# Kernel tuning notes

Measured on AMD Instinct MI355X. Metric: run time of the kernel, lower is better.

## Reference

```python
import jax, jax.numpy as jnp
import numpy as np

VOCAB = 1500   # vocab_size
NE = 208       # n_embed
T = 256        # block_size
NH = 4         # n_head
HD = NE // NH  # head_size = 52
NL = 8         # n_layer
B = 256        # batch


def setup_inputs() -> dict:
    key = jax.random.key(0)
    ks = jax.random.split(key, 16)
    f = lambda k, shape: jax.random.normal(k, shape, jnp.float32) * 0.02
    return {
        "idx": jax.random.randint(ks[0], (B, T), 0, VOCAB),
        "targets": jax.random.randint(ks[1], (B, T), 0, VOCAB),
        "tok_emb": f(ks[2], (VOCAB, NE)),
        "pos_emb": f(ks[3], (T, NE)),
        # per-layer stacked attention params (separate no-bias Q/K/V Linears per head)
        "Wq": f(ks[4], (NL, NH, NE, HD)),
        "Wk": f(ks[5], (NL, NH, NE, HD)),
        "Wv": f(ks[6], (NL, NH, NE, HD)),
        "Wo": f(ks[7], (NL, NE, NE)),
        "bo": jnp.zeros((NL, NE), jnp.float32),
        "ln1_g": jnp.ones((NL, NE), jnp.float32),
        "ln1_b": jnp.zeros((NL, NE), jnp.float32),
        "W1": f(ks[8], (NL, NE, 4 * NE)),
        "b1": jnp.zeros((NL, 4 * NE), jnp.float32),
        "W2": f(ks[9], (NL, 4 * NE, NE)),
        "b2": jnp.zeros((NL, NE), jnp.float32),
        "ln2_g": jnp.ones((NL, NE), jnp.float32),
        "ln2_b": jnp.zeros((NL, NE), jnp.float32),
        "lnf_g": jnp.ones((NE,), jnp.float32),
        "lnf_b": jnp.zeros((NE,), jnp.float32),
        "Wlm": f(ks[10], (NE, VOCAB)),
        "blm": jnp.zeros((VOCAB,), jnp.float32),
    }


def _layernorm(x, g, b, eps=1e-5):
    mu = x.mean(-1, keepdims=True)
    var = ((x - mu) ** 2).mean(-1, keepdims=True)
    return (x - mu) * jax.lax.rsqrt(var + eps) * g + b


def reference(idx, targets, tok_emb, pos_emb, Wq, Wk, Wv, Wo, bo,
              ln1_g, ln1_b, W1, b1, W2, b2, ln2_g, ln2_b,
              lnf_g, lnf_b, Wlm, blm):
    x = tok_emb[idx] + pos_emb[None, :, :]          # [B, T, NE]
    mask = jnp.tril(jnp.ones((T, T), bool))
    scale = NE ** -0.5                               # NOTE: scales by n_embed, per source (C**-0.5)
    for i in range(NL):
        h = _layernorm(x, ln1_g[i], ln1_b[i])
        q = jnp.einsum('btc,hcd->bhtd', h, Wq[i])
        k = jnp.einsum('btc,hcd->bhtd', h, Wk[i])
        v = jnp.einsum('btc,hcd->bhtd', h, Wv[i])
        s = jnp.einsum('bhtd,bhsd->bhts', q, k) * scale
        s = jnp.where(mask, s, -jnp.inf)
        a = jax.nn.softmax(s, axis=-1)               # dropout is identity in eval
        o = jnp.einsum('bhts,bhsd->bhtd', a, v)
        o = o.transpose(0, 2, 1, 3).reshape(x.shape[0], T, NE)
        x = x + o @ Wo[i] + bo[i]
        h2 = _layernorm(x, ln2_g[i], ln2_b[i])
        x = x + jax.nn.relu(h2 @ W1[i] + b1[i]) @ W2[i] + b2[i]
    x = _layernorm(x, lnf_g, lnf_b)
    logits = (x @ Wlm + blm).reshape(-1, VOCAB)      # [B*T, VOCAB]
    logp = jax.nn.log_softmax(logits, axis=-1)
    loss = -jnp.take_along_axis(logp, targets.reshape(-1, 1), axis=-1).mean()
    return logits, loss
```

## Files before the change

### kernel.cpp

```cpp
#include <hip/hip_runtime.h>
#include <hip/hip_bf16.h>
#include <math.h>

#define VOCAB 1500
#define NE    208
#define TT    256
#define NHD   4
#define HD    52
#define NL    8
#define BBATCH 256
#define NTOK  (BBATCH * TT)
#define KP    224

typedef __attribute__((ext_vector_type(8))) short bf16x8;
typedef __attribute__((ext_vector_type(4))) short s16x4;
typedef __attribute__((ext_vector_type(4))) float f32x4;
typedef __attribute__((ext_vector_type(4))) _Float16 f16x4;

__device__ __forceinline__ void gload16(const void* g, void* l) {
  __builtin_amdgcn_global_load_lds(
      (const __attribute__((address_space(1))) unsigned int*)g,
      (__attribute__((address_space(3))) unsigned int*)l, 16, 0, 0);
}
__device__ __forceinline__ float bf2f(short u) {
  union { unsigned int i; float f; } cv;
  cv.i = ((unsigned int)(unsigned short)u) << 16;
  return cv.f;
}

#define P_QKV 1146880
#define P_O   458752
#define P_1   1605632
#define P_2   1703936
#define P_LM  344064
__global__ __launch_bounds__(256) void k_prep_all(const float* __restrict__ Wq,
                                                  const float* __restrict__ Wk,
                                                  const float* __restrict__ Wv,
                                                  const float* __restrict__ Wo,
                                                  const float* __restrict__ W1,
                                                  const float* __restrict__ W2,
                                                  const float* __restrict__ Wlm,
                                                  __hip_bfloat16* __restrict__ qkvT,
                                                  __hip_bfloat16* __restrict__ oT,
                                                  __hip_bfloat16* __restrict__ t1,
                                                  __hip_bfloat16* __restrict__ t2,
                                                  __hip_bfloat16* __restrict__ lmT) {
  int gi = blockIdx.x * 256 + threadIdx.x;
  if (gi < P_QKV) {
    int i = gi;
    int c = i % KP;
    int jl = i / KP;
    int j = jl % 640, l = jl / 640;
    float v = 0.f;
    if (j < 624 && c < NE) {
      int sel = j / NE, hd = j - sel * NE;
      int h = hd / HD, d = hd - h * HD;
      const float* W = (sel == 0) ? Wq : (sel == 1) ? Wk : Wv;
      v = W[(((size_t)l * NHD + h) * NE + c) * HD + d];
    }
    qkvT[i] = __float2bfloat16(v);
  } else if (gi < P_QKV + P_O) {
    int i = gi - P_QKV;
    int c = i % KP;
    int jl = i / KP;
    int j = jl % 256, l = jl / 256;
    float v = (j < NE && c < NE) ? Wo[((size_t)l * NE + c) * NE + j] : 0.f;
    oT[i] = __float2bfloat16(v);
  } else if (gi < P_QKV + P_O + P_1) {
    int i = gi - (P_QKV + P_O);
    int c = i % KP;
    int jl = i / KP;
    int j = jl % 896, l = jl / 896;
    float v = (j < 832 && c < NE) ? W1[((size_t)l * NE + c) * 832 + j] : 0.f;
    t1[i] = __float2bfloat16(v);
  } else if (gi < P_QKV + P_O + P_1 + P_2) {
    int i = gi - (P_QKV + P_O + P_1);
    int c = i % 832;
    int jl = i / 832;
    int j = jl % 256, l = jl / 256;
    float v = (j < NE) ? W2[((size_t)l * 832 + c) * NE + j] : 0.f;
    t2[i] = __float2bfloat16(v);
  } else {
    int i = gi - (P_QKV + P_O + P_1 + P_2);
    int c = i % KP;
    int j = i / KP;
    float v = (j < VOCAB && c < NE) ? Wlm[(size_t)c * VOCAB + j] : 0.f;
    lmT[i] = __float2bfloat16(v);
  }
}

__global__ __launch_bounds__(256) void k_embed_ln(const int* __restrict__ idx,
                                                  const float* __restrict__ tok,
                                                  const float* __restrict__ pos,
                                                  const float* __restrict__ g,
                                                  const float* __restrict__ b,
                                                  __hip_bfloat16* __restrict__ x,
                                                  __hip_bfloat16* __restrict__ h) {
  int r = blockIdx.x * 4 + (threadIdx.x >> 6);
  int lane = threadIdx.x & 63;
  const int c0 = lane * 4;
  const int t = r & (TT - 1);
  float v[4] = {0.f, 0.f, 0.f, 0.f};
  float s = 0.f;
  if (lane < 52) {
    float4 tv = *(const float4*)(tok + (size_t)idx[r] * NE + c0);
    float4 pv = *(const float4*)(pos + (size_t)t * NE + c0);
    v[0] = tv.x + pv.x; v[1] = tv.y + pv.y;
    v[2] = tv.z + pv.z; v[3] = tv.w + pv.w;
    s = v[0] + v[1] + v[2] + v[3];
  }
  #pragma unroll
  for (int o = 32; o; o >>= 1) s += __shfl_xor(s, o);
  float mu = s * (1.f / NE);
  float q = 0.f;
  if (lane < 52) {
    #pragma unroll
    for (int i = 0; i < 4; i++) { float d = v[i] - mu; q += d * d; }
  }
  #pragma unroll
  for (int o = 32; o; o >>= 1) q += __shfl_xor(q, o);
  float inv = rsqrtf(q * (1.f / NE) + 1e-5f);
  if (lane < 52) {
    s16x4 xv;
    #pragma unroll
    for (int i = 0; i < 4; i++)
      xv[i] = (short)__bfloat16_as_ushort(__float2bfloat16(v[i]));
    *(s16x4*)(x + (size_t)r * NE + c0) = xv;
  }
  if (lane < 56) {
    s16x4 outv = {};
    if (lane < 52) {
      #pragma unroll
      for (int i = 0; i < 4; i++) {
        float o = (v[i] - mu) * inv * g[c0 + i] + b[c0 + i];
        outv[i] = (short)__bfloat16_as_ushort(__float2bfloat16(o));
      }
    }
    *(s16x4*)(h + (size_t)r * KP + c0) = outv;
  }
}

template <bool RELU, bool RESID, bool BIAS, bool OUTBF, bool EXPSUM>
__global__ __launch_bounds__(256) void k_mgemm(const __hip_bfloat16* __restrict__ A, int lda,
                                               const __hip_bfloat16* __restrict__ BT, int ldb,
                                               const float* __restrict__ bias,
                                               const __hip_bfloat16* __restrict__ resid,
                                               void* __restrict__ Cout, int ldc,
                                               int N, int K,
                                               float* __restrict__ esum) {
  __shared__ __hip_bfloat16 As[2][128 * 32];
  __shared__ __hip_bfloat16 Bs[2][128 * 32];
  const int gx = gridDim.x;
  const int id = blockIdx.x + gx * blockIdx.y;
  const int qq = (gx * gridDim.y) >> 3;
  const int wid2 = (id & 7) * qq + (id >> 3);
  const int by = wid2 / gx, bx = wid2 - by * gx;
  const int bm = by * 128, bn = bx * 128;
  const int tid = threadIdx.x;
  const int wave = tid >> 6, lane = tid & 63;
  const int wr = (wave >> 1) * 64, wc = (wave & 1) * 64;
  const int l15 = lane & 15, l4 = lane >> 4;
  const int srow = tid >> 2, sgrp = (tid & 3) * 8;
  const int srow2 = srow + 64;
  f32x4 acc[4][4] = {};
  const int nt = K / 32;
  gload16(A + (size_t)(bm + srow) * lda + sgrp, &As[0][tid * 8]);
  gload16(BT + (size_t)(bn + srow) * ldb + sgrp, &Bs[0][tid * 8]);
  gload16(A + (size_t)(bm + srow2) * lda + sgrp, &As[0][(256 + tid) * 8]);
  gload16(BT + (size_t)(bn + srow2) * ldb + sgrp, &Bs[0][(256 + tid) * 8]);
  int cur = 0;
  for (int t = 0; t < nt; t++) {
    if (t + 1 < nt) {
      int k1 = (t + 1) * 32;
      gload16(A + (size_t)(bm + srow) * lda + k1 + sgrp, &As[cur ^ 1][tid * 8]);
      gload16(BT + (size_t)(bn + srow) * ldb + k1 + sgrp, &Bs[cur ^ 1][tid * 8]);
      gload16(A + (size_t)(bm + srow2) * lda + k1 + sgrp, &As[cur ^ 1][(256 + tid) * 8]);
      gload16(BT + (size_t)(bn + srow2) * ldb + k1 + sgrp, &Bs[cur ^ 1][(256 + tid) * 8]);
      asm volatile("s_waitcnt vmcnt(4)" ::: "memory");
    } else {
      asm volatile("s_waitcnt vmcnt(0)" ::: "memory");
    }
    __builtin_amdgcn_s_barrier();
    bf16x8 af[4], bfr[4];
    #pragma unroll
    for (int m = 0; m < 4; m++)
      af[m] = *(const bf16x8*)&As[cur][(wr + m * 16 + l15) * 32 + l4 * 8];
    #pragma unroll
    for (int n = 0; n < 4; n++)
      bfr[n] = *(const bf16x8*)&Bs[cur][(wc + n * 16 + l15) * 32 + l4 * 8];
    #pragma unroll
    for (int m = 0; m < 4; m++)
      #pragma unroll
      for (int n = 0; n < 4; n++)
        acc[m][n] = __builtin_amdgcn_mfma_f32_16x16x32_bf16(af[m], bfr[n], acc[m][n], 0, 0, 0);
    if (t + 1 < nt) __builtin_amdgcn_s_barrier();
    cur ^= 1;
  }
  float es[4][4];
  if (EXPSUM) {
    #pragma unroll
    for (int m = 0; m < 4; m++)
      #pragma unroll
      for (int j = 0; j < 4; j++) es[m][j] = 0.f;
  }
  #pragma unroll
  for (int m = 0; m < 4; m++) {
    #pragma unroll
    for (int n = 0; n < 4; n++) {
      int col = bn + wc + n * 16 + l15;
      if (col < N) {
        float bv = BIAS ? bias[col] : 0.f;
        #pragma unroll
        for (int j = 0; j < 4; j++) {
          int row = bm + wr + m * 16 + l4 * 4 + j;
          float v = acc[m][n][j] + bv;
          if (RELU) v = fmaxf(v, 0.f);
          size_t off = (size_t)row * ldc + col;
          if (RESID) v += __bfloat162float(resid[off]);
          if (OUTBF) ((__hip_bfloat16*)Cout)[off] = __float2bfloat16(v);
          else       ((float*)Cout)[off] = v;
          if (EXPSUM) es[m][j] += __expf(v);
        }
      }
    }
  }
  if (EXPSUM) {
    #pragma unroll
    for (int m = 0; m < 4; m++)
      #pragma unroll
      for (int j = 0; j < 4; j++) {
        float e = es[m][j];
        #pragma unroll
        for (int off = 1; off < 16; off <<= 1) e += __shfl_xor(e, off);
        if (l15 == 0) {
          int row = bm + wr + m * 16 + l4 * 4 + j;
          esum[(size_t)row * 24 + bx * 2 + (wave & 1)] = e;
        }
      }
  }
}

__global__ __launch_bounds__(512) void k_mgemm_ln(const __hip_bfloat16* __restrict__ A, int lda,
                                                  const __hip_bfloat16* __restrict__ BT, int ldb,
                                                  const float* __restrict__ bias,
                                                  const __hip_bfloat16* __restrict__ resid,
                                                  const float* __restrict__ g,
                                                  const float* __restrict__ bb,
                                                  __hip_bfloat16* __restrict__ xout,
                                                  __hip_bfloat16* __restrict__ hout,
                                                  int K) {
  __shared__ __hip_bfloat16 As[2][128 * 32];
  __shared__ __hip_bfloat16 Bs[2][256 * 32];
  __shared__ float red[128][4];
  const int bm = blockIdx.x * 128;
  const int tid = threadIdx.x;
  const int wid = tid >> 6, lane = tid & 63;
  const int wr = (wid >> 1) * 32, wc = (wid & 1) * 128;
  const int l15 = lane & 15, l4 = lane >> 4;
  const int srow = tid >> 2, sgrp = (tid & 3) * 8;
  f32x4 acc[2][8] = {};
  const int nt = K / 32;
  gload16(A + (size_t)(bm + srow) * lda + sgrp, &As[0][tid * 8]);
  gload16(BT + (size_t)srow * ldb + sgrp, &Bs[0][tid * 8]);
  gload16(BT + (size_t)(128 + srow) * ldb + sgrp, &Bs[0][(512 + tid) * 8]);
  int cur = 0;
  for (int t = 0; t < nt; t++) {
    if (t + 1 < nt) {
      int k1 = (t + 1) * 32;
      gload16(A + (size_t)(bm + srow) * lda + k1 + sgrp, &As[cur ^ 1][tid * 8]);
      gload16(BT + (size_t)srow * ldb + k1 + sgrp, &Bs[cur ^ 1][tid * 8]);
      gload16(BT + (size_t)(128 + srow) * ldb + k1 + sgrp, &Bs[cur ^ 1][(512 + tid) * 8]);
      asm volatile("s_waitcnt vmcnt(3)" ::: "memory");
    } else {
      asm volatile("s_waitcnt vmcnt(0)" ::: "memory");
    }
    __builtin_amdgcn_s_barrier();
    bf16x8 af[2], bfr[8];
    #pragma unroll
    for (int m = 0; m < 2; m++)
      af[m] = *(const bf16x8*)&As[cur][(wr + m * 16 + l15) * 32 + l4 * 8];
    #pragma unroll
    for (int n = 0; n < 8; n++)
      bfr[n] = *(const bf16x8*)&Bs[cur][(wc + n * 16 + l15) * 32 + l4 * 8];
    #pragma unroll
    for (int m = 0; m < 2; m++)
      #pragma unroll
      for (int n = 0; n < 8; n++)
        acc[m][n] = __builtin_amdgcn_mfma_f32_16x16x32_bf16(af[m], bfr[n], acc[m][n], 0, 0, 0);
    if (t + 1 < nt) __builtin_amdgcn_s_barrier();
    cur ^= 1;
  }
  #pragma unroll
  for (int m = 0; m < 2; m++)
    #pragma unroll
    for (int n = 0; n < 8; n++) {
      int col = wc + n * 16 + l15;
      #pragma unroll
      for (int j = 0; j < 4; j++) {
        int row = bm + wr + m * 16 + l4 * 4 + j;
        float v = 0.f;
        if (col < NE)
          v = acc[m][n][j] + bias[col] + __bfloat162float(resid[(size_t)row * NE + col]);
        acc[m][n][j] = v;
      }
    }
  #pragma unroll
  for (int m = 0; m < 2; m++)
    #pragma unroll
    for (int j = 0; j < 4; j++) {
      float s = 0.f, q = 0.f;
      #pragma unroll
      for (int n = 0; n < 8; n++) { float v = acc[m][n][j]; s += v; q += v * v; }
      #pragma unroll
      for (int off = 1; off < 16; off <<= 1) {
        s += __shfl_xor(s, off);
        q += __shfl_xor(q, off);
      }
      if (l15 == 0) {
        int row = wr + m * 16 + l4 * 4 + j;
        red[row][(wid & 1) * 2 + 0] = s;
        red[row][(wid & 1) * 2 + 1] = q;
      }
    }
  __syncthreads();
  #pragma unroll
  for (int m = 0; m < 2; m++)
    #pragma unroll
    for (int j = 0; j < 4; j++) {
      int lrow = wr + m * 16 + l4 * 4 + j;
      float s = red[lrow][0] + red[lrow][2];
      float q = red[lrow][1] + red[lrow][3];
      float mu = s * (1.f / NE);
      float var = q * (1.f / NE) - mu * mu;
      float inv = rsqrtf(var + 1e-5f);
      size_t row = bm + lrow;
      #pragma unroll
      for (int n = 0; n < 8; n++) {
        int col = wc + n * 16 + l15;
        if (col < NE) {
          float v = acc[m][n][j];
          xout[row * NE + col] = __float2bfloat16(v);
          hout[row * KP + col] = __float2bfloat16((v - mu) * inv * g[col] + bb[col]);
        } else if (col < KP) {
          hout[row * KP + col] = __float2bfloat16(0.f);
        }
      }
    }
}

#define KSTRIDE 64
#define VSTRIDE 260
__global__ __launch_bounds__(256) void k_attn_mfma(const __hip_bfloat16* __restrict__ qkv,
                                                   __hip_bfloat16* __restrict__ o) {
  __shared__ __hip_bfloat16 Ks[256 * KSTRIDE];
  __shared__ _Float16      Vt[64 * VSTRIDE];
  const int bh0 = blockIdx.x;
  const int bh = (bh0 & 7) * 128 + (bh0 >> 3);
  const int b = bh >> 2, h = bh & 3;
  const __hip_bfloat16* base = qkv + (size_t)b * TT * 624;
  const int tid = threadIdx.x;
  #pragma unroll
  for (int it = 0; it < 16; it++) {
    int u = it * 256 + tid;
    int t = u >> 4, d4 = (u & 15) * 4;
    s16x4 v = {};
    if (d4 < 52) v = *(const s16x4*)(base + t * 624 + 208 + h * HD + d4);
    *(s16x4*)&Ks[t * KSTRIDE + d4] = v;
  }
  #pragma unroll
  for (int it = 0; it < 13; it++) {
    int slot = it * 256 + tid;
    int t = slot / 13, dl = (slot - t * 13) * 4;
    s16x4 kv = *(const s16x4*)(base + t * 624 + 416 + h * HD + dl);
    #pragma unroll
    for (int i = 0; i < 4; i++)
      Vt[(dl + i) * VSTRIDE + t] = (_Float16)bf2f(kv[i]);
  }
  #pragma unroll
  for (int it = 0; it < 12; it++)
    Vt[(52 + it) * VSTRIDE + tid] = (_Float16)0.f;
  __syncthreads();

  const int w = tid >> 6, lane = tid & 63, l15 = lane & 15, l4 = lane >> 4;
  const float scale = 0.06933752453f;
  const int qts[4] = {w, 7 - w, 8 + w, 15 - w};
  bf16x8 qf[4][2];
  #pragma unroll
  for (int i = 0; i < 4; i++) {
    const __hip_bfloat16* qrow = base + (qts[i] * 16 + l15) * 624 + h * HD;
    #pragma unroll
    for (int ks = 0; ks < 2; ks++) {
      int s = ks * 32 + l4 * 8;
      union { s16x4 h2[2]; bf16x8 v; } u;
      u.h2[0] = (s <= 48) ? *(const s16x4*)(qrow + s) : (s16x4){};
      u.h2[1] = (s <= 44) ? *(const s16x4*)(qrow + s + 4) : (s16x4){};
      qf[i][ks] = u.v;
    }
  }
  f32x4 oacc[4][4] = {};
  float mrun[4] = {-1e30f, -1e30f, -1e30f, -1e30f};
  float lrun[4] = {0.f, 0.f, 0.f, 0.f};
  const int cmax = 15 - w;
  for (int c = 0; c <= cmax; c++) {
    const int kb = c * 16;
    const bf16x8 kf0 = *(const bf16x8*)&Ks[(kb + l15) * KSTRIDE + l4 * 8];
    const bf16x8 kf1 = *(const bf16x8*)&Ks[(kb + l15) * KSTRIDE + 32 + l4 * 8];
    #pragma unroll
    for (int i = 0; i < 4; i++) {
      if (qts[i] < c) continue;
      __builtin_amdgcn_s_setprio(1);
      f32x4 s4 = __builtin_amdgcn_mfma_f32_16x16x32_bf16(kf0, qf[i][0],
                                                         (f32x4){0.f, 0.f, 0.f, 0.f}, 0, 0, 0);
      s4 = __builtin_amdgcn_mfma_f32_16x16x32_bf16(kf1, qf[i][1], s4, 0, 0, 0);
      __builtin_amdgcn_s_setprio(0);
      const int q = qts[i] * 16 + l15;
      float pv[4];
      float pmax = -1e30f;
      #pragma unroll
      for (int j = 0; j < 4; j++) {
        int key = kb + l4 * 4 + j;
        float s = s4[j] * scale;
        pv[j] = (key <= q) ? s : -1e30f;
        pmax = fmaxf(pmax, pv[j]);
      }
      pmax = fmaxf(pmax, __shfl_xor(pmax, 16));
      pmax = fmaxf(pmax, __shfl_xor(pmax, 32));
      if (!__all(pmax - mrun[i] <= 8.f)) {
        const float newm = fmaxf(mrun[i], pmax);
        const float r = __expf(mrun[i] - newm);
        lrun[i] *= r;
        mrun[i] = newm;
        #pragma unroll
        for (int m = 0; m < 4; m++) {
          oacc[m][i][0] *= r; oacc[m][i][1] *= r;
          oacc[m][i][2] *= r; oacc[m][i][3] *= r;
        }
      }
      float psum = 0.f;
      f16x4 pb;
      #pragma unroll
      for (int j = 0; j < 4; j++) {
        float e = __expf(pv[j] - mrun[i]);
        psum += e;
        pb[j] = (_Float16)e;
      }
      psum += __shfl_xor(psum, 16);
      psum += __shfl_xor(psum, 32);
      lrun[i] += psum;
      __builtin_amdgcn_s_setprio(1);
      #pragma unroll
      for (int m = 0; m < 4; m++) {
        f16x4 vf = *(const f16x4*)&Vt[(m * 16 + l15) * VSTRIDE + kb + l4 * 4];
        oacc[m][i] = __builtin_amdgcn_mfma_f32_16x16x16f16(vf, pb, oacc[m][i], 0, 0, 0);
      }
      __builtin_amdgcn_s_setprio(0);
    }
  }
  #pragma unroll
  for (int i = 0; i < 4; i++) {
    const float inv = 1.f / lrun[i];
    __hip_bfloat16* orow = o + (size_t)(b * TT + qts[i] * 16 + l15) * KP + h * HD;
    #pragma unroll
    for (int m = 0; m < 4; m++)
      #pragma unroll
      for (int j = 0; j < 4; j++) {
        int d = m * 16 + l4 * 4 + j;
        if (d < HD) orow[d] = __float2bfloat16(oacc[m][i][j] * inv);
      }
  }
}

__global__ __launch_bounds__(256) void k_loss_fin(const float* __restrict__ esum,
                                                  const float* __restrict__ logits,
                                                  const int* __restrict__ targets,
                                                  float* __restrict__ row_loss) {
  int r = blockIdx.x * 256 + threadIdx.x;
  const float* e = esum + (size_t)r * 24;
  float s = 0.f;
  #pragma unroll
  for (int i = 0; i < 24; i++) s += e[i];
  row_loss[r] = __logf(s) - logits[(size_t)r * VOCAB + targets[r]];
}

__global__ __launch_bounds__(256) void k_loss_reduce(const float* __restrict__ row_loss,
                                                     float* __restrict__ out_loss) {
  __shared__ float sh[256];
  float s = 0.f;
  for (int i = threadIdx.x; i < NTOK; i += 256) s += row_loss[i];
  sh[threadIdx.x] = s;
  __syncthreads();
  for (int k = 128; k; k >>= 1) {
    if (threadIdx.x < k) sh[threadIdx.x] += sh[threadIdx.x + k];
    __syncthreads();
  }
  if (threadIdx.x == 0) *out_loss = sh[0] * (1.f / NTOK);
}

extern "C" void kernel_launch(void* const* d_in, const int* in_sizes, int n_in,
                              void* d_out, int out_size, void* d_ws, size_t ws_size,
                              hipStream_t stream) {
  const int*   idx     = (const int*)d_in[0];
  const int*   targets = (const int*)d_in[1];
  const float* tok     = (const float*)d_in[2];
  const float* pos     = (const float*)d_in[3];
  const float* Wq      = (const float*)d_in[4];
  const float* Wk      = (const float*)d_in[5];
  const float* Wv      = (const float*)d_in[6];
  const float* Wo      = (const float*)d_in[7];
  const float* bo      = (const float*)d_in[8];
  const float* ln1g    = (const float*)d_in[9];
  const float* ln1b    = (const float*)d_in[10];
  const float* W1      = (const float*)d_in[11];
  const float* b1      = (const float*)d_in[12];
  const float* W2      = (const float*)d_in[13];
  const float* b2      = (const float*)d_in[14];
  const float* ln2g    = (const float*)d_in[15];
  const float* ln2b    = (const float*)d_in[16];
  const float* lnfg    = (const float*)d_in[17];
  const float* lnfb    = (const float*)d_in[18];
  const float* Wlm     = (const float*)d_in[19];
  const float* blm     = (const float*)d_in[20];
  float* out = (float*)d_out;

  char* w = (char*)d_ws;
  __hip_bfloat16* x   = (__hip_bfloat16*)w; w += (size_t)NTOK * NE * 2;
  __hip_bfloat16* qkv = (__hip_bfloat16*)w; w += (size_t)NTOK * 624 * 2;
  __hip_bfloat16* hbf = (__hip_bfloat16*)w; w += (size_t)NTOK * KP * 2;
  __hip_bfloat16* act = (__hip_bfloat16*)w; w += (size_t)NTOK * 832 * 2;
  __hip_bfloat16* WqkvT = (__hip_bfloat16*)w; w += (size_t)P_QKV * 2;
  __hip_bfloat16* WoT   = (__hip_bfloat16*)w; w += (size_t)P_O * 2;
  __hip_bfloat16* W1T   = (__hip_bfloat16*)w; w += (size_t)P_1 * 2;
  __hip_bfloat16* W2T   = (__hip_bfloat16*)w; w += (size_t)P_2 * 2;
  __hip_bfloat16* WlmT  = (__hip_bfloat16*)w; w += (size_t)P_LM * 2;
  float* row_loss = (float*)w;              w += (size_t)NTOK * 4;
  float* esum     = (float*)w;

  k_prep_all<<<(P_QKV + P_O + P_1 + P_2 + P_LM) / 256, 256, 0, stream>>>(
      Wq, Wk, Wv, Wo, W1, W2, Wlm, WqkvT, WoT, W1T, W2T, WlmT);
  k_embed_ln<<<NTOK / 4, 256, 0, stream>>>(idx, tok, pos, ln1g, ln1b, x, hbf);

  for (int l = 0; l < NL; l++) {
    k_mgemm<false, false, false, true, false><<<dim3(5, 512), 256, 0, stream>>>(
        hbf, KP, WqkvT + (size_t)l * 640 * KP, KP, nullptr, nullptr, qkv, 624, 624, KP, nullptr);
    k_attn_mfma<<<BBATCH * NHD, 256, 0, stream>>>(qkv, hbf);
    k_mgemm_ln<<<512, 512, 0, stream>>>(
        hbf, KP, WoT + (size_t)l * 256 * KP, KP, bo + l * NE, x,
        ln2g + l * NE, ln2b + l * NE, x, hbf, KP);
    k_mgemm<true, false, true, true, false><<<dim3(7, 512), 256, 0, stream>>>(
        hbf, KP, W1T + (size_t)l * 896 * KP, KP, b1 + l * 832, nullptr, act, 832, 832, KP, nullptr);
    const float* gn = (l < NL - 1) ? (ln1g + (l + 1) * NE) : lnfg;
    const float* bn = (l < NL - 1) ? (ln1b + (l + 1) * NE) : lnfb;
    k_mgemm_ln<<<512, 512, 0, stream>>>(
        act, 832, W2T + (size_t)l * 256 * 832, 832, b2 + l * NE, x,
        gn, bn, x, hbf, 832);
  }

  k_mgemm<false, false, true, false, true><<<dim3(12, 512), 256, 0, stream>>>(
      hbf, KP, WlmT, KP, blm, nullptr, out, VOCAB, VOCAB, KP, esum);

  k_loss_fin<<<NTOK / 256, 256, 0, stream>>>(esum, out, targets, row_loss);
  k_loss_reduce<<<1, 256, 0, stream>>>(row_loss, out + ((size_t)out_size - 1));
}
```

Before: 2.442 ms.

## Fuse MLP up-projection, ReLU and down-projection with residual LayerNorm

Replaces the separate W1 GEMM and the W2 GEMM+LayerNorm with one kernel. Each 128-row block computes 64-column chunks of the hidden activation into shared memory and immediately accumulates them into the W2 output, so the 832-wide activation tensor never goes to global memory. It also vectorises the attention output stores to 4-element packed writes and removes the unused RESID template path. The fused kernel runs with one block per row tile and synchronises several times per chunk with no double-buffering of W1, which may reduce overlap and occupancy compared with the separate GEMMs.

```diff
diff --git a/kernel.cpp b/kernel.cpp
--- a/kernel.cpp
+++ b/kernel.cpp
@@ -15,6 +15,7 @@
 typedef __attribute__((ext_vector_type(8))) short bf16x8;
 typedef __attribute__((ext_vector_type(4))) short s16x4;
 typedef __attribute__((ext_vector_type(4))) float f32x4;
+typedef __attribute__((ext_vector_type(4))) int i32x4;
 typedef __attribute__((ext_vector_type(4))) _Float16 f16x4;
 
 __device__ __forceinline__ void gload16(const void* g, void* l) {
@@ -26,6 +27,9 @@
   union { unsigned int i; float f; } cv;
   cv.i = ((unsigned int)(unsigned short)u) << 16;
   return cv.f;
+}
+__device__ __forceinline__ short f2bf(float f) {
+  return (short)__bfloat16_as_ushort(__float2bfloat16(f));
 }
 
 #define P_QKV 1146880
@@ -123,28 +127,24 @@
   if (lane < 52) {
     s16x4 xv;
     #pragma unroll
-    for (int i = 0; i < 4; i++)
-      xv[i] = (short)__bfloat16_as_ushort(__float2bfloat16(v[i]));
+    for (int i = 0; i < 4; i++) xv[i] = f2bf(v[i]);
     *(s16x4*)(x + (size_t)r * NE + c0) = xv;
   }
   if (lane < 56) {
     s16x4 outv = {};
     if (lane < 52) {
       #pragma unroll
-      for (int i = 0; i < 4; i++) {
-        float o = (v[i] - mu) * inv * g[c0 + i] + b[c0 + i];
-        outv[i] = (short)__bfloat16_as_ushort(__float2bfloat16(o));
-      }
+      for (int i = 0; i < 4; i++)
+        outv[i] = f2bf((v[i] - mu) * inv * g[c0 + i] + b[c0 + i]);
     }
     *(s16x4*)(h + (size_t)r * KP + c0) = outv;
   }
 }
 
-template <bool RELU, bool RESID, bool BIAS, bool OUTBF, bool EXPSUM>
+template <bool RELU, bool BIAS, bool OUTBF, bool EXPSUM>
 __global__ __launch_bounds__(256) void k_mgemm(const __hip_bfloat16* __restrict__ A, int lda,
                                                const __hip_bfloat16* __restrict__ BT, int ldb,
                                                const float* __restrict__ bias,
-                                               const __hip_bfloat16* __restrict__ resid,
                                                void* __restrict__ Cout, int ldc,
                                                int N, int K,
                                                float* __restrict__ esum) {
@@ -216,7 +216,6 @@
           float v = acc[m][n][j] + bv;
           if (RELU) v = fmaxf(v, 0.f);
           size_t off = (size_t)row * ldc + col;
-          if (RESID) v += __bfloat162float(resid[off]);
           if (OUTBF) ((__hip_bfloat16*)Cout)[off] = __float2bfloat16(v);
           else       ((float*)Cout)[off] = v;
           if (EXPSUM) es[m][j] += __expf(v);
@@ -348,6 +347,132 @@
     }
 }
 
+__global__ __launch_bounds__(512) void k_mlp_ln(const __hip_bfloat16* __restrict__ h,
+                                                const __hip_bfloat16* __restrict__ W1T,
+                                                const float* __restrict__ b1,
+                                                const __hip_bfloat16* __restrict__ W2T,
+                                                const float* __restrict__ b2,
+                                                const float* __restrict__ g,
+                                                const float* __restrict__ bb,
+                                                __hip_bfloat16* __restrict__ xio,
+                                                __hip_bfloat16* __restrict__ hout) {
+  __shared__ __hip_bfloat16 Hs[128 * 232];
+  __shared__ __hip_bfloat16 W1s[64 * 224];
+  __shared__ __hip_bfloat16 Ac[128 * 72];
+  __shared__ __hip_bfloat16 W2s[2][256 * 32];
+  __shared__ float sred[128][4], qred[128][4];
+  const int bm = blockIdx.x * 128;
+  const int tid = threadIdx.x;
+  const int wid = tid >> 6, lane = tid & 63;
+  const int l15 = lane & 15, l4 = lane >> 4;
+  const int w1r = (wid >> 1) * 32, w1c = (wid & 1) * 32;
+  const int w2r = (wid >> 2) * 64, w2c = (wid & 3) * 64;
+  #pragma unroll
+  for (int it = 0; it < 14; it++) {
+    int slot = it * 512 + tid;
+    int row = slot / 56, gq = slot - row * 56;
+    *(s16x4*)&Hs[row * 232 + gq * 4] =
+        *(const s16x4*)(h + (size_t)(bm + row) * KP + gq * 4);
+  }
+  f32x4 acc2[4][4] = {};
+  for (int jc = 0; jc < 13; jc++) {
+    for (int s = tid; s < 1792; s += 512)
+      gload16(W1T + (size_t)(jc * 64 + s / 28) * KP + (s % 28) * 8, &W1s[s * 8]);
+    __syncthreads();
+    f32x4 acc1[2][2] = {};
+    #pragma unroll
+    for (int kt = 0; kt < 7; kt++) {
+      bf16x8 a0 = *(const bf16x8*)&Hs[(w1r + l15) * 232 + kt * 32 + l4 * 8];
+      bf16x8 a1 = *(const bf16x8*)&Hs[(w1r + 16 + l15) * 232 + kt * 32 + l4 * 8];
+      bf16x8 c0 = *(const bf16x8*)&W1s[(w1c + l15) * 224 + kt * 32 + l4 * 8];
+      bf16x8 c1 = *(const bf16x8*)&W1s[(w1c + 16 + l15) * 224 + kt * 32 + l4 * 8];
+      acc1[0][0] = __builtin_amdgcn_mfma_f32_16x16x32_bf16(a0, c0, acc1[0][0], 0, 0, 0);
+      acc1[0][1] = __builtin_amdgcn_mfma_f32_16x16x32_bf16(a0, c1, acc1[0][1], 0, 0, 0);
+      acc1[1][0] = __builtin_amdgcn_mfma_f32_16x16x32_bf16(a1, c0, acc1[1][0], 0, 0, 0);
+      acc1[1][1] = __builtin_amdgcn_mfma_f32_16x16x32_bf16(a1, c1, acc1[1][1], 0, 0, 0);
+    }
+    #pragma unroll
+    for (int m = 0; m < 2; m++)
+      #pragma unroll
+      for (int n = 0; n < 2; n++) {
+        int colL = w1c + n * 16 + l15;
+        float bv = b1[jc * 64 + colL];
+        #pragma unroll
+        for (int j = 0; j < 4; j++) {
+          int rowL = w1r + m * 16 + l4 * 4 + j;
+          Ac[rowL * 72 + colL] = __float2bfloat16(fmaxf(acc1[m][n][j] + bv, 0.f));
+        }
+      }
+    __syncthreads();
+    #pragma unroll
+    for (int kt2 = 0; kt2 < 2; kt2++) {
+      for (int s = tid; s < 1024; s += 512)
+        gload16(W2T + (size_t)(s >> 2) * 832 + jc * 64 + kt2 * 32 + (s & 3) * 8,
+                &W2s[kt2][s * 8]);
+      __syncthreads();
+      bf16x8 af[4], bfr[4];
+      #pragma unroll
+      for (int m = 0; m < 4; m++)
+        af[m] = *(const bf16x8*)&Ac[(w2r + m * 16 + l15) * 72 + kt2 * 32 + l4 * 8];
+      #pragma unroll
+      for (int n = 0; n < 4; n++)
+        bfr[n] = *(const bf16x8*)&W2s[kt2][(w2c + n * 16 + l15) * 32 + l4 * 8];
+      #pragma unroll
+      for (int m = 0; m < 4; m++)
+        #pragma unroll
+        for (int n = 0; n < 4; n++)
+          acc2[m][n] = __builtin_amdgcn_mfma_f32_16x16x32_bf16(af[m], bfr[n], acc2[m][n], 0, 0, 0);
+    }
+  }
+  #pragma unroll
+  for (int m2 = 0; m2 < 4; m2++)
+    #pragma unroll
+    for (int j = 0; j < 4; j++) {
+      int rowL = w2r + m2 * 16 + l4 * 4 + j;
+      float s = 0.f, q = 0.f;
+      #pragma unroll
+      for (int n2 = 0; n2 < 4; n2++) {
+        int col = w2c + n2 * 16 + l15;
+        float v = 0.f;
+        if (col < NE)
+          v = acc2[m2][n2][j] + b2[col] +
+              __bfloat162float(xio[(size_t)(bm + rowL) * NE + col]);
+        acc2[m2][n2][j] = v;
+        s += v; q += v * v;
+      }
+      #pragma unroll
+      for (int off = 1; off < 16; off <<= 1) {
+        s += __shfl_xor(s, off);
+        q += __shfl_xor(q, off);
+      }
+      if (l15 == 0) { sred[rowL][wid & 3] = s; qred[rowL][wid & 3] = q; }
+    }
+  __syncthreads();
+  #pragma unroll
+  for (int m2 = 0; m2 < 4; m2++)
+    #pragma unroll
+    for (int j = 0; j < 4; j++) {
+      int rowL = w2r + m2 * 16 + l4 * 4 + j;
+      float s = sred[rowL][0] + sred[rowL][1] + sred[rowL][2] + sred[rowL][3];
+      float q = qred[rowL][0] + qred[rowL][1] + qred[rowL][2] + qred[rowL][3];
+      float mu = s * (1.f / NE);
+      float var = q * (1.f / NE) - mu * mu;
+      float inv = rsqrtf(var + 1e-5f);
+      size_t row = bm + rowL;
+      #pragma unroll
+      for (int n2 = 0; n2 < 4; n2++) {
+        int col = w2c + n2 * 16 + l15;
+        if (col < NE) {
+          float v = acc2[m2][n2][j];
+          xio[row * NE + col] = __float2bfloat16(v);
+          hout[row * KP + col] = __float2bfloat16((v - mu) * inv * g[col] + bb[col]);
+        } else if (col < KP) {
+          hout[row * KP + col] = __float2bfloat16(0.f);
+        }
+      }
+    }
+}
+
 #define KSTRIDE 64
 #define VSTRIDE 260
 __global__ __launch_bounds__(256) void k_attn_mfma(const __hip_bfloat16* __restrict__ qkv,
@@ -461,12 +586,15 @@
     const float inv = 1.f / lrun[i];
     __hip_bfloat16* orow = o + (size_t)(b * TT + qts[i] * 16 + l15) * KP + h * HD;
     #pragma unroll
-    for (int m = 0; m < 4; m++)
-      #pragma unroll
-      for (int j = 0; j < 4; j++) {
-        int d = m * 16 + l4 * 4 + j;
-        if (d < HD) orow[d] = __float2bfloat16(oacc[m][i][j] * inv);
-      }
+    for (int m = 0; m < 4; m++) {
+      int d0 = m * 16 + l4 * 4;
+      if (d0 + 3 < HD) {
+        s16x4 pk;
+        #pragma unroll
+        for (int j = 0; j < 4; j++) pk[j] = f2bf(oacc[m][i][j] * inv);
+        *(s16x4*)(orow + d0) = pk;
+      }
+    }
   }
 }
 
@@ -527,6 +655,7 @@
   __hip_bfloat16* qkv = (__hip_bfloat16*)w; w += (size_t)NTOK * 624 * 2;
   __hip_bfloat16* hbf = (__hip_bfloat16*)w; w += (size_t)NTOK * KP * 2;
   __hip_bfloat16* act = (__hip_bfloat16*)w; w += (size_t)NTOK * 832 * 2;
+  (void)act;
   __hip_bfloat16* WqkvT = (__hip_bfloat16*)w; w += (size_t)P_QKV * 2;
   __hip_bfloat16* WoT   = (__hip_bfloat16*)w; w += (size_t)P_O * 2;
   __hip_bfloat16* W1T   = (__hip_bfloat16*)w; w += (size_t)P_1 * 2;
@@ -540,23 +669,21 @@
   k_embed_ln<<<NTOK / 4, 256, 0, stream>>>(idx, tok, pos, ln1g, ln1b, x, hbf);
 
   for (int l = 0; l < NL; l++) {
-    k_mgemm<false, false, false, true, false><<<dim3(5, 512), 256, 0, stream>>>(
-        hbf, KP, WqkvT + (size_t)l * 640 * KP, KP, nullptr, nullptr, qkv, 624, 624, KP, nullptr);
+    k_mgemm<false, false, true, false><<<dim3(5, 512), 256, 0, stream>>>(
+        hbf, KP, WqkvT + (size_t)l * 640 * KP, KP, nullptr, qkv, 624, 624, KP, nullptr);
     k_attn_mfma<<<BBATCH * NHD, 256, 0, stream>>>(qkv, hbf);
     k_mgemm_ln<<<512, 512, 0, stream>>>(
         hbf, KP, WoT + (size_t)l * 256 * KP, KP, bo + l * NE, x,
         ln2g + l * NE, ln2b + l * NE, x, hbf, KP);
-    k_mgemm<true, false, true, true, false><<<dim3(7, 512), 256, 0, stream>>>(
-        hbf, KP, W1T + (size_t)l * 896 * KP, KP, b1 + l * 832, nullptr, act, 832, 832, KP, nullptr);
     const float* gn = (l < NL - 1) ? (ln1g + (l + 1) * NE) : lnfg;
     const float* bn = (l < NL - 1) ? (ln1b + (l + 1) * NE) : lnfb;
-    k_mgemm_ln<<<512, 512, 0, stream>>>(
-        act, 832, W2T + (size_t)l * 256 * 832, 832, b2 + l * NE, x,
-        gn, bn, x, hbf, 832);
-  }
-
-  k_mgemm<false, false, true, false, true><<<dim3(12, 512), 256, 0, stream>>>(
-      hbf, KP, WlmT, KP, blm, nullptr, out, VOCAB, VOCAB, KP, esum);
+    k_mlp_ln<<<512, 512, 0, stream>>>(
+        hbf, W1T + (size_t)l * 896 * KP, b1 + l * 832,
+        W2T + (size_t)l * 256 * 832, b2 + l * NE, gn, bn, x, hbf);
+  }
+
+  k_mgemm<false, true, false, true><<<dim3(12, 512), 256, 0, stream>>>(
+      hbf, KP, WlmT, KP, blm, out, VOCAB, VOCAB, KP, esum);
 
   k_loss_fin<<<NTOK / 256, 256, 0, stream>>>(esum, out, targets, row_loss);
   k_loss_reduce<<<1, 256, 0, stream>>>(row_loss, out + ((size_t)out_size - 1));
```

New measurement: 2.353 ms. 3.7% less time.
